# Kernel optimization log

Hardware: AMD Instinct MI355X
Metric: run time of the kernel (lower is better)

## Reference

```python
import jax, jax.numpy as jnp
import numpy as np

NUM_TOKENS = 4096
LATENT_DIM = 128
BETA = 0.25
TEMP = 1.0  # temperature buffer (eval mode, no annealing)


def _l2_normalize(x, eps=1e-12):
    n = jnp.linalg.norm(x, axis=-1, keepdims=True)
    return x / jnp.maximum(n, eps)


def setup_inputs() -> dict:
    key = jax.random.key(0)
    k1, k2 = jax.random.split(key)
    latent = jax.random.normal(k1, (16, 1024, LATENT_DIM), dtype=jnp.float32)
    # codebook init: uniform(-1/num_tokens, 1/num_tokens) as in the module
    codebook_w = jax.random.uniform(
        k2, (NUM_TOKENS, LATENT_DIM), dtype=jnp.float32,
        minval=-1.0 / NUM_TOKENS, maxval=1.0 / NUM_TOKENS)
    return {"latent": latent, "codebook_w": codebook_w}


def reference(latent, codebook_w):
    B, S, D = latent.shape
    K = codebook_w.shape[0]
    flat = latent.reshape(-1, D)                      # [N, D]
    N = flat.shape[0]

    # cosine similarity between normalized inputs and codes
    cos = _l2_normalize(flat) @ _l2_normalize(codebook_w).T  # [N, K]

    # squared euclidean distances
    dist = (jnp.sum(flat * flat, axis=1, keepdims=True)
            - 2.0 * (flat @ codebook_w.T)
            + jnp.sum(codebook_w * codebook_w, axis=1))       # [N, K]

    soft = jax.nn.softmax(-dist / max(TEMP, 1e-5), axis=-1)   # [N, K]
    idx = jnp.argmax(soft, axis=-1)                            # [N]
    hard = jax.nn.one_hot(idx, K, dtype=flat.dtype)            # [N, K]
    # straight-through assignment
    assign = hard + soft - jax.lax.stop_gradient(soft)

    sel_cos = jnp.take_along_axis(cos, idx[:, None], axis=1).mean()

    # codebook self pairwise euclidean distances (K x K)
    sq = jnp.sum(codebook_w * codebook_w, axis=1)
    d2 = sq[:, None] + sq[None, :] - 2.0 * (codebook_w @ codebook_w.T)
    d = jnp.sqrt(jnp.maximum(d2, 0.0))
    # diagonal is exactly 0 after clamp, so off-diagonal mean = sum/(K*(K-1))
    avg_euclidean = d.sum() / (K * (K - 1))
    min_euclidean = jnp.min(jnp.where(jnp.eye(K, dtype=bool), jnp.inf, d))

    quantized = (assign @ codebook_w).reshape(B, S, D)
    commitment_loss = BETA * jnp.mean((jax.lax.stop_gradient(latent) - quantized) ** 2)
    codebook_loss = jnp.mean((latent - jax.lax.stop_gradient(quantized)) ** 2)
    quantized_st = latent + jax.lax.stop_gradient(quantized - latent)

    avg_probs = hard.mean(axis=0)
    perplexity = jnp.exp(-jnp.sum(avg_probs * jnp.log(avg_probs + 1e-10)))

    return (quantized_st, idx, commitment_loss, codebook_loss,
            perplexity, sel_cos, avg_euclidean, min_euclidean)
```

## Files before the change

### kernel.cpp

```cpp
#include <hip/hip_runtime.h>
#include <hip/hip_fp16.h>
#include <math.h>

#define NTOK 16384
#define KCB  4096
#define DIM  128
#define NG8  (KCB / 8)

typedef short bf16x8 __attribute__((ext_vector_type(8)));
typedef float f32x4  __attribute__((ext_vector_type(4)));

static __device__ inline unsigned short rne_bf16(float f) {
  unsigned u = __float_as_uint(f);
  return (unsigned short)((u + 0x7FFFu + ((u >> 16) & 1u)) >> 16);
}


__global__ __launch_bounds__(256) void k_prep(const float* __restrict__ lat,
                                              const float* __restrict__ cb,
                                              float* __restrict__ sumx2,
                                              float* __restrict__ sumc2,
                                              float* __restrict__ absum,
                                              int* __restrict__ cnt,
                                              unsigned short* __restrict__ cbh) {
  if (blockIdx.x < (NTOK + KCB) / 4) {
    if (blockIdx.x < 16) cnt[blockIdx.x * 256 + threadIdx.x] = 0;
    const int row  = blockIdx.x * 4 + (threadIdx.x >> 6);
    const int lane = threadIdx.x & 63;
    const float* src = (row < NTOK) ? (lat + (size_t)row * DIM)
                                    : (cb + (size_t)(row - NTOK) * DIM);
    float2 v = *(const float2*)(src + lane * 2);
    double s  = (double)v.x * (double)v.x + (double)v.y * (double)v.y;
    double sa = fabs((double)v.x) + fabs((double)v.y);
#pragma unroll
    for (int m = 32; m >= 1; m >>= 1) {
      s  += __shfl_xor(s, m, 64);
      sa += __shfl_xor(sa, m, 64);
    }
    if (lane == 0) {
      if (row < NTOK) { sumx2[row] = (float)s; absum[row] = (float)sa; }
      else            sumc2[row - NTOK] = (float)s;
    }
  } else {
    const int b = blockIdx.x - (NTOK + KCB) / 4;
    const int base = (b * 256 + threadIdx.x) * 8;
    float4 v0 = *(const float4*)(cb + base);
    float4 v1 = *(const float4*)(cb + base + 4);
    ushort4 o0, o1;
    o0.x = rne_bf16(v0.x); o0.y = rne_bf16(v0.y); o0.z = rne_bf16(v0.z); o0.w = rne_bf16(v0.w);
    o1.x = rne_bf16(v1.x); o1.y = rne_bf16(v1.y); o1.z = rne_bf16(v1.z); o1.w = rne_bf16(v1.w);
    *(ushort4*)(cbh + base) = o0;
    *(ushort4*)(cbh + base + 4) = o1;
  }
}

__global__ __launch_bounds__(256) void k_approx(const float* __restrict__ lat,
                                                const unsigned short* __restrict__ cbh,
                                                unsigned short* __restrict__ gmax8) {
  __shared__ __align__(16) unsigned char smem[16384];
  __shared__ __align__(16) unsigned short gbuf[256][36];
  const int t = threadIdx.x;
  const int w = t >> 6, l = t & 63;
  const int l15 = l & 15, lq = l >> 4;
  const int tokb = blockIdx.x * 256 + w * 64;
  const int ct0 = blockIdx.y * 4;

  bf16x8 bfr[4][4];
#pragma unroll
  for (int ctile = 0; ctile < 4; ++ctile) {
    const float* row = lat + (size_t)(tokb + ctile * 16 + l15) * DIM;
#pragma unroll
    for (int ks = 0; ks < 4; ++ks) {
      const int d0 = ks * 32 + lq * 4;
      float4 c0 = *(const float4*)(row + d0);
      float4 c1 = *(const float4*)(row + d0 + 16);
      union { ushort4 u4[2]; bf16x8 v; } cv;
      cv.u4[0].x = rne_bf16(c0.x); cv.u4[0].y = rne_bf16(c0.y);
      cv.u4[0].z = rne_bf16(c0.z); cv.u4[0].w = rne_bf16(c0.w);
      cv.u4[1].x = rne_bf16(c1.x); cv.u4[1].y = rne_bf16(c1.y);
      cv.u4[1].z = rne_bf16(c1.z); cv.u4[1].w = rne_bf16(c1.w);
      bfr[ctile][ks] = cv.v;
    }
  }

  for (int it = 0; it < 4; ++it) {
    const int ct = ct0 + it;
    __syncthreads();
    {
      const int r = t & 63, seg = t >> 6;
      const unsigned short* src = cbh + (size_t)(ct * 64 + r) * DIM + seg * 32;
      const int sw = (r & 7) << 4;
#pragma unroll
      for (int i = 0; i < 4; ++i) {
        uint4 v = *(const uint4*)(src + i * 8);
        *(uint4*)(smem + r * 256 + ((seg * 64 + i * 16) ^ sw)) = v;
      }
    }
    __syncthreads();

#pragma unroll
    for (int rt = 0; rt < 4; ++rt) {
      const int row = rt * 16 + l15;
      const int sw = (row & 7) << 4;
      bf16x8 afr[4];
#pragma unroll
      for (int ks = 0; ks < 4; ++ks) {
        const int off = ks * 64 + lq * 8;
        union { uint2 u2[2]; bf16x8 v; } cv;
        cv.u2[0] = *(const uint2*)(smem + row * 256 + (off ^ sw));
        cv.u2[1] = *(const uint2*)(smem + row * 256 + (((off + 32)) ^ sw));
        afr[ks] = cv.v;
      }
      f32x4 acc[4];
#pragma unroll
      for (int c = 0; c < 4; ++c) acc[c] = (f32x4){0.0f, 0.0f, 0.0f, 0.0f};
#pragma unroll
      for (int ks = 0; ks < 4; ++ks)
#pragma unroll
        for (int c = 0; c < 4; ++c)
          acc[c] = __builtin_amdgcn_mfma_f32_16x16x32_bf16(afr[ks], bfr[c][ks], acc[c], 0, 0, 0);
#pragma unroll
      for (int c = 0; c < 4; ++c) {
        float gm = fmaxf(fmaxf(acc[c][0], acc[c][1]), fmaxf(acc[c][2], acc[c][3]));
        gm = fmaxf(gm, __shfl_xor(gm, 16, 64));
        if ((lq & 1) == 0) {
          const int tokl = w * 64 + c * 16 + l15;
          gbuf[tokl][it * 8 + rt * 2 + (lq >> 1)] =
              __half_as_ushort(__float2half(gm));
        }
      }
    }
  }

  __syncthreads();
  for (int c = t; c < 1024; c += 256) {
    const int token = c >> 2, seg = c & 3;
    uint2 a = *(const uint2*)(&gbuf[token][seg * 8]);
    uint2 b = *(const uint2*)(&gbuf[token][seg * 8 + 4]);
    uint4 o = make_uint4(a.x, a.y, b.x, b.y);
    *(uint4*)(gmax8 + (size_t)(blockIdx.x * 256 + token) * NG8 +
              blockIdx.y * 32 + seg * 8) = o;
  }
}

__global__ __launch_bounds__(256) void k_resolve_pair(
    const float* __restrict__ lat,
    const float* __restrict__ cb,
    const float* __restrict__ sumx2,
    const float* __restrict__ sumc2,
    const float* __restrict__ absum,
    const unsigned short* __restrict__ gmax8,
    const unsigned short* __restrict__ cbh,
    float* __restrict__ qout,
    float* __restrict__ idx_out,
    float* __restrict__ msum,
    float* __restrict__ csum,
    int* __restrict__ cnt,
    float* __restrict__ pairsum,
    float* __restrict__ pairmin) {
  __shared__ __align__(16) unsigned char pool[16640];

  if (blockIdx.x < 1024) {
    const int f = blockIdx.x;
    const int bx = f & 15, by = f >> 4;
    unsigned char* smem = pool;
    float* qs = (float*)(pool + 16384);
    const int t = threadIdx.x;
    const int w = t >> 6, l = t & 63;
    const int l15 = l & 15, lq = l >> 4;
    const int jb = bx * 256 + w * 64;
    const int kb = by * 64;

    {
      const int r = t & 63, seg = t >> 6;
      const unsigned short* src = cbh + (size_t)(kb + r) * DIM + seg * 32;
      const int sw = (r & 7) << 4;
#pragma unroll
      for (int i = 0; i < 4; ++i) {
        uint4 v = *(const uint4*)(src + i * 8);
        *(uint4*)(smem + r * 256 + ((seg * 64 + i * 16) ^ sw)) = v;
      }
      if (t < 64) qs[t] = sumc2[kb + t];
    }

    bf16x8 bfr[4][4];
    float qj[4];
#pragma unroll
    for (int ct = 0; ct < 4; ++ct) {
      const unsigned short* rh = cbh + (size_t)(jb + ct * 16 + l15) * DIM;
#pragma unroll
      for (int ks = 0; ks < 4; ++ks) {
        const int d0 = ks * 32 + lq * 4;
        union { ushort4 u4[2]; bf16x8 v; } cvv;
        cvv.u4[0] = *(const ushort4*)(rh + d0);
        cvv.u4[1] = *(const ushort4*)(rh + d0 + 16);
        bfr[ct][ks] = cvv.v;
      }
      qj[ct] = sumc2[jb + ct * 16 + l15];
    }
    __syncthreads();

    float lsum = 0.0f, lmin = INFINITY;

#pragma unroll
    for (int rt = 0; rt < 4; ++rt) {
      const int row = rt * 16 + l15;
      const int sw = (row & 7) << 4;
      bf16x8 afr[4];
#pragma unroll
      for (int ks = 0; ks < 4; ++ks) {
        const int off = ks * 64 + lq * 8;
        union { uint2 u2[2]; bf16x8 v; } cv;
        cv.u2[0] = *(const uint2*)(smem + row * 256 + (off ^ sw));
        cv.u2[1] = *(const uint2*)(smem + row * 256 + (((off + 32)) ^ sw));
        afr[ks] = cv.v;
      }
      f32x4 acc[4];
#pragma unroll
      for (int c = 0; c < 4; ++c) acc[c] = (f32x4){0.0f, 0.0f, 0.0f, 0.0f};
#pragma unroll
      for (int ks = 0; ks < 4; ++ks)
#pragma unroll
        for (int c = 0; c < 4; ++c)
          acc[c] = __builtin_amdgcn_mfma_f32_16x16x32_bf16(afr[ks], bfr[c][ks], acc[c], 0, 0, 0);

#pragma unroll
      for (int c = 0; c < 4; ++c) {
        const int jg = jb + c * 16 + l15;
#pragma unroll
        for (int reg = 0; reg < 4; ++reg) {
          const int krl = rt * 16 + lq * 4 + reg;
          const int kg = kb + krl;
          const float d2 = (qj[c] + qs[krl]) - 2.0f * acc[c][reg];
          const float dd = sqrtf(fmaxf(d2, 0.0f));
          lsum += dd;
          if (jg != kg) lmin = fminf(lmin, dd);
        }
      }
    }

#pragma unroll
    for (int s = 32; s >= 1; s >>= 1) {
      lsum += __shfl_xor(lsum, s, 64);
      lmin = fminf(lmin, __shfl_xor(lmin, s, 64));
    }
    if (l == 0) {
      const int slot = f * 4 + w;
      pairsum[slot] = lsum;
      pairmin[slot] = lmin;
    }
  } else {
    const int bid = blockIdx.x - 1024;
    float (*xs)[DIM] = (float (*)[DIM])pool;
    unsigned short (*q)[NG8] = (unsigned short (*)[NG8])(pool + 2048);
    const int w = threadIdx.x >> 6, l = threadIdx.x & 63;
    const int tok = bid * 4 + w;

    const float2 xv = *(const float2*)(lat + (size_t)tok * DIM + l * 2);
    const uint4 hv = *(const uint4*)(gmax8 + (size_t)tok * NG8 + l * 8);
    const float sx = sumx2[tok];
    const float ab = absum[tok];
    *(float2*)(&xs[w][l * 2]) = xv;

    float hf[8];
    hf[0] = __half2float(__ushort_as_half((unsigned short)(hv.x & 0xFFFFu)));
    hf[1] = __half2float(__ushort_as_half((unsigned short)(hv.x >> 16)));
    hf[2] = __half2float(__ushort_as_half((unsigned short)(hv.y & 0xFFFFu)));
    hf[3] = __half2float(__ushort_as_half((unsigned short)(hv.y >> 16)));
    hf[4] = __half2float(__ushort_as_half((unsigned short)(hv.z & 0xFFFFu)));
    hf[5] = __half2float(__ushort_as_half((unsigned short)(hv.z >> 16)));
    hf[6] = __half2float(__ushort_as_half((unsigned short)(hv.w & 0xFFFFu)));
    hf[7] = __half2float(__ushort_as_half((unsigned short)(hv.w >> 16)));
    float m = hf[0];
#pragma unroll
    for (int i = 1; i < 8; ++i) m = fmaxf(m, hf[i]);
#pragma unroll
    for (int s = 32; s >= 1; s >>= 1) m = fmaxf(m, __shfl_xor(m, s, 64));
    const float thr = m - (ab * 3.8224e-6f + 6.0e-5f);

    const unsigned long long ltm = (1ull << l) - 1ull;
    int n = 0;
#pragma unroll
    for (int i = 0; i < 8; ++i) {
      const bool f2 = (hf[i] >= thr);
      const unsigned long long b = __ballot(f2);
      if (f2) q[w][n + __popcll(b & ltm)] = (unsigned short)(l * 8 + i);
      n += __popcll(b);
    }

    const int slot = l >> 3, cidx = l & 7;
    unsigned long long bestp = ~0ull;
    const float4* xr4 = (const float4*)xs[w];

    for (int base = 0; base < n; base += 8) {
      unsigned long long pack = ~0ull;
      const int qi = base + slot;
      if (qi < n) {
        const int g = (int)q[w][qi];
        const int code = g * 8 + cidx;
        const float4* crow = (const float4*)(cb + (size_t)code * DIM);
        float acc = 0.0f;
#pragma unroll 8
        for (int ch = 0; ch < 32; ++ch) {
          const float4 c = crow[ch];
          const float4 x = xr4[ch];
          acc = fmaf(x.x, c.x, acc); acc = fmaf(x.y, c.y, acc);
          acc = fmaf(x.z, c.z, acc); acc = fmaf(x.w, c.w, acc);
        }
        const float dist = (sx - 2.0f * acc) + sumc2[code];
        pack = ((unsigned long long)__float_as_uint(dist) << 32) | (unsigned)code;
      }
#pragma unroll
      for (int s = 32; s >= 1; s >>= 1) {
        const unsigned long long o = __shfl_xor(pack, s, 64);
        pack = (o < pack) ? o : pack;
      }
      bestp = (pack < bestp) ? pack : bestp;
    }

    const int code = (int)(bestp & 0xFFFFFFFFull);
    const float2 c2 = *(const float2*)(cb + (size_t)code * DIM + l * 2);
    const float o0 = xv.x + (c2.x - xv.x);
    const float o1 = xv.y + (c2.y - xv.y);
    *(float2*)(qout + (size_t)tok * DIM + l * 2) = make_float2(o0, o1);
    const float e0 = xv.x - c2.x, e1 = xv.y - c2.y;
    float msel = e0 * e0 + e1 * e1;
    float dt = xv.x * c2.x + xv.y * c2.y;
#pragma unroll
    for (int s = 32; s >= 1; s >>= 1) {
      msel += __shfl_xor(msel, s, 64);
      dt += __shfl_xor(dt, s, 64);
    }
    if (l == 0) {
      const float nx = fmaxf(sqrtf(sx), 1e-12f);
      const float nc = fmaxf(sqrtf(sumc2[code]), 1e-12f);
      msum[tok] = msel;
      csum[tok] = dt / (nx * nc);
      idx_out[tok] = (float)code;
      atomicAdd(&cnt[code], 1);
    }
  }
}

__global__ __launch_bounds__(1024) void k_final(const int* __restrict__ cnt,
                                                const float* __restrict__ msum,
                                                const float* __restrict__ csum,
                                                const float* __restrict__ pairsum,
                                                const float* __restrict__ pairmin,
                                                float* __restrict__ outs) {
  __shared__ float sh[1024], sh2[1024], sh3[1024], sh4[1024];
  const int t = threadIdx.x;
  float ent = 0.0f;
  for (int k = t; k < KCB; k += 1024) {
    const float p = (float)cnt[k] * (1.0f / (float)NTOK);
    ent += p * logf(p + 1e-10f);
  }
  float ms = 0.0f, cs = 0.0f;
  for (int i = t; i < NTOK; i += 1024) { ms += msum[i]; cs += csum[i]; }
  float ps = 0.0f, pm = INFINITY;
  for (int i = t; i < 4096; i += 1024) { ps += pairsum[i]; pm = fminf(pm, pairmin[i]); }

  sh[t] = ent; sh2[t] = ms; sh3[t] = cs; sh4[t] = ps;
  __syncthreads();
  for (int s = 512; s >= 1; s >>= 1) {
    if (t < s) { sh[t] += sh[t + s]; sh2[t] += sh2[t + s];
                 sh3[t] += sh3[t + s]; sh4[t] += sh4[t + s]; }
    __syncthreads();
  }
  const float ent_tot = sh[0];
  const float ms_tot  = sh2[0];
  const float cs_tot  = sh3[0];
  const float ps_tot  = sh4[0];
  __syncthreads();
  sh[t] = pm;
  __syncthreads();
  for (int s = 512; s >= 1; s >>= 1) {
    if (t < s) sh[t] = fminf(sh[t], sh[t + s]);
    __syncthreads();
  }
  if (t == 0) {
    const float mse = ms_tot * (1.0f / (float)(NTOK * DIM));
    outs[0] = 0.25f * mse;
    outs[1] = mse;
    outs[2] = expf(-ent_tot);
    outs[3] = cs_tot * (1.0f / (float)NTOK);
    outs[4] = ps_tot / ((float)KCB * (float)(KCB - 1));
    outs[5] = sh[0];
  }
}

extern "C" void kernel_launch(void* const* d_in, const int* in_sizes, int n_in,
                              void* d_out, int out_size, void* d_ws, size_t ws_size,
                              hipStream_t stream) {
  const float* lat = (const float*)d_in[0];
  const float* cb  = (const float*)d_in[1];

  float* out     = (float*)d_out;
  float* qout    = out;
  float* idx_out = out + (size_t)NTOK * DIM;
  float* outs    = idx_out + NTOK;

  float* W        = (float*)d_ws;
  float* sumx2    = W;
  float* sumc2    = sumx2 + NTOK;
  float* absum    = sumc2 + KCB;
  int*   cnt      = (int*)(absum + NTOK);
  float* msum     = (float*)(cnt + KCB);
  float* csum     = msum + NTOK;
  float* pairsum  = csum + NTOK;
  float* pairmin  = pairsum + 4096;
  unsigned short* cbh   = (unsigned short*)(pairmin + 4096);
  unsigned short* gmax8 = cbh + (size_t)KCB * DIM;

  hipLaunchKernelGGL(k_prep, dim3((NTOK + KCB) / 4 + KCB * DIM / (256 * 8)),
                     dim3(256), 0, stream, lat, cb, sumx2, sumc2, absum, cnt, cbh);
  hipLaunchKernelGGL(k_approx, dim3(NTOK / 256, 16), dim3(256), 0, stream,
                     lat, cbh, gmax8);
  hipLaunchKernelGGL(k_resolve_pair, dim3(1024 + NTOK / 4), dim3(256), 0, stream,
                     lat, cb, sumx2, sumc2, absum, gmax8, cbh,
                     qout, idx_out, msum, csum, cnt, pairsum, pairmin);
  hipLaunchKernelGGL(k_final, dim3(1), dim3(1024), 0, stream, cnt,
                     msum, csum, pairsum, pairmin, outs);
}
```

Measured before the change: 120.4 us.

## Fuse prep and approx kernels, convert codebook to bf16 on the fly

Merges the norm/prep kernel and the bf16 approximate-scan kernel into one launch, with the norm blocks appended after the 1024 MFMA scan blocks. The separate bf16 codebook copy (cbh) is dropped; both the scan and the resolve/pair kernels now read the fp32 codebook and round to bf16 while staging into shared memory or registers. This removes one kernel launch, the dependency barrier between prep and scan, and a codebook write and read. The cost is twice the global bytes per codebook load plus repeated conversion ALU work in every block.

```diff
diff --git a/kernel.cpp b/kernel.cpp
--- a/kernel.cpp
+++ b/kernel.cpp
@@ -16,16 +16,109 @@
 }
 
 
-__global__ __launch_bounds__(256) void k_prep(const float* __restrict__ lat,
+__global__ __launch_bounds__(256) void k_scan(const float* __restrict__ lat,
                                               const float* __restrict__ cb,
                                               float* __restrict__ sumx2,
                                               float* __restrict__ sumc2,
                                               float* __restrict__ absum,
                                               int* __restrict__ cnt,
-                                              unsigned short* __restrict__ cbh) {
-  if (blockIdx.x < (NTOK + KCB) / 4) {
-    if (blockIdx.x < 16) cnt[blockIdx.x * 256 + threadIdx.x] = 0;
-    const int row  = blockIdx.x * 4 + (threadIdx.x >> 6);
+                                              unsigned short* __restrict__ gmax8) {
+  __shared__ __align__(16) unsigned char smem[16384];
+  __shared__ __align__(16) unsigned short gbuf[256][36];
+  if (blockIdx.x < 1024) {
+    const int xb = blockIdx.x & 63, yb = blockIdx.x >> 6;
+    const int t = threadIdx.x;
+    const int w = t >> 6, l = t & 63;
+    const int l15 = l & 15, lq = l >> 4;
+    const int tokb = xb * 256 + w * 64;
+    const int ct0 = yb * 4;
+
+    bf16x8 bfr[4][4];
+#pragma unroll
+    for (int ctile = 0; ctile < 4; ++ctile) {
+      const float* row = lat + (size_t)(tokb + ctile * 16 + l15) * DIM;
+#pragma unroll
+      for (int ks = 0; ks < 4; ++ks) {
+        const int d0 = ks * 32 + lq * 4;
+        float4 c0 = *(const float4*)(row + d0);
+        float4 c1 = *(const float4*)(row + d0 + 16);
+        union { ushort4 u4[2]; bf16x8 v; } cv;
+        cv.u4[0].x = rne_bf16(c0.x); cv.u4[0].y = rne_bf16(c0.y);
+        cv.u4[0].z = rne_bf16(c0.z); cv.u4[0].w = rne_bf16(c0.w);
+        cv.u4[1].x = rne_bf16(c1.x); cv.u4[1].y = rne_bf16(c1.y);
+        cv.u4[1].z = rne_bf16(c1.z); cv.u4[1].w = rne_bf16(c1.w);
+        bfr[ctile][ks] = cv.v;
+      }
+    }
+
+    for (int it = 0; it < 4; ++it) {
+      const int ct = ct0 + it;
+      __syncthreads();
+      {
+        const int r = t & 63, seg = t >> 6;
+        const float* src = cb + (size_t)(ct * 64 + r) * DIM + seg * 32;
+        const int sw = (r & 7) << 4;
+#pragma unroll
+        for (int i = 0; i < 4; ++i) {
+          float4 a = *(const float4*)(src + i * 8);
+          float4 b = *(const float4*)(src + i * 8 + 4);
+          union { unsigned short s[8]; uint4 v; } pk;
+          pk.s[0] = rne_bf16(a.x); pk.s[1] = rne_bf16(a.y);
+          pk.s[2] = rne_bf16(a.z); pk.s[3] = rne_bf16(a.w);
+          pk.s[4] = rne_bf16(b.x); pk.s[5] = rne_bf16(b.y);
+          pk.s[6] = rne_bf16(b.z); pk.s[7] = rne_bf16(b.w);
+          *(uint4*)(smem + r * 256 + ((seg * 64 + i * 16) ^ sw)) = pk.v;
+        }
+      }
+      __syncthreads();
+
+#pragma unroll
+      for (int rt = 0; rt < 4; ++rt) {
+        const int row = rt * 16 + l15;
+        const int sw = (row & 7) << 4;
+        bf16x8 afr[4];
+#pragma unroll
+        for (int ks = 0; ks < 4; ++ks) {
+          const int off = ks * 64 + lq * 8;
+          union { uint2 u2[2]; bf16x8 v; } cv;
+          cv.u2[0] = *(const uint2*)(smem + row * 256 + (off ^ sw));
+          cv.u2[1] = *(const uint2*)(smem + row * 256 + (((off + 32)) ^ sw));
+          afr[ks] = cv.v;
+        }
+        f32x4 acc[4];
+#pragma unroll
+        for (int c = 0; c < 4; ++c) acc[c] = (f32x4){0.0f, 0.0f, 0.0f, 0.0f};
+#pragma unroll
+        for (int ks = 0; ks < 4; ++ks)
+#pragma unroll
+          for (int c = 0; c < 4; ++c)
+            acc[c] = __builtin_amdgcn_mfma_f32_16x16x32_bf16(afr[ks], bfr[c][ks], acc[c], 0, 0, 0);
+#pragma unroll
+        for (int c = 0; c < 4; ++c) {
+          float gm = fmaxf(fmaxf(acc[c][0], acc[c][1]), fmaxf(acc[c][2], acc[c][3]));
+          gm = fmaxf(gm, __shfl_xor(gm, 16, 64));
+          if ((lq & 1) == 0) {
+            const int tokl = w * 64 + c * 16 + l15;
+            gbuf[tokl][it * 8 + rt * 2 + (lq >> 1)] =
+                __half_as_ushort(__float2half(gm));
+          }
+        }
+      }
+    }
+
+    __syncthreads();
+    for (int c = t; c < 1024; c += 256) {
+      const int token = c >> 2, seg = c & 3;
+      uint2 a = *(const uint2*)(&gbuf[token][seg * 8]);
+      uint2 b = *(const uint2*)(&gbuf[token][seg * 8 + 4]);
+      uint4 o = make_uint4(a.x, a.y, b.x, b.y);
+      *(uint4*)(gmax8 + (size_t)(xb * 256 + token) * NG8 +
+                yb * 32 + seg * 8) = o;
+    }
+  } else {
+    const int rb = blockIdx.x - 1024;
+    if (rb < 16) cnt[rb * 256 + threadIdx.x] = 0;
+    const int row  = rb * 4 + (threadIdx.x >> 6);
     const int lane = threadIdx.x & 63;
     const float* src = (row < NTOK) ? (lat + (size_t)row * DIM)
                                     : (cb + (size_t)(row - NTOK) * DIM);
@@ -41,105 +134,6 @@
       if (row < NTOK) { sumx2[row] = (float)s; absum[row] = (float)sa; }
       else            sumc2[row - NTOK] = (float)s;
     }
-  } else {
-    const int b = blockIdx.x - (NTOK + KCB) / 4;
-    const int base = (b * 256 + threadIdx.x) * 8;
-    float4 v0 = *(const float4*)(cb + base);
-    float4 v1 = *(const float4*)(cb + base + 4);
-    ushort4 o0, o1;
-    o0.x = rne_bf16(v0.x); o0.y = rne_bf16(v0.y); o0.z = rne_bf16(v0.z); o0.w = rne_bf16(v0.w);
-    o1.x = rne_bf16(v1.x); o1.y = rne_bf16(v1.y); o1.z = rne_bf16(v1.z); o1.w = rne_bf16(v1.w);
-    *(ushort4*)(cbh + base) = o0;
-    *(ushort4*)(cbh + base + 4) = o1;
-  }
-}
-
-__global__ __launch_bounds__(256) void k_approx(const float* __restrict__ lat,
-                                                const unsigned short* __restrict__ cbh,
-                                                unsigned short* __restrict__ gmax8) {
-  __shared__ __align__(16) unsigned char smem[16384];
-  __shared__ __align__(16) unsigned short gbuf[256][36];
-  const int t = threadIdx.x;
-  const int w = t >> 6, l = t & 63;
-  const int l15 = l & 15, lq = l >> 4;
-  const int tokb = blockIdx.x * 256 + w * 64;
-  const int ct0 = blockIdx.y * 4;
-
-  bf16x8 bfr[4][4];
-#pragma unroll
-  for (int ctile = 0; ctile < 4; ++ctile) {
-    const float* row = lat + (size_t)(tokb + ctile * 16 + l15) * DIM;
-#pragma unroll
-    for (int ks = 0; ks < 4; ++ks) {
-      const int d0 = ks * 32 + lq * 4;
-      float4 c0 = *(const float4*)(row + d0);
-      float4 c1 = *(const float4*)(row + d0 + 16);
-      union { ushort4 u4[2]; bf16x8 v; } cv;
-      cv.u4[0].x = rne_bf16(c0.x); cv.u4[0].y = rne_bf16(c0.y);
-      cv.u4[0].z = rne_bf16(c0.z); cv.u4[0].w = rne_bf16(c0.w);
-      cv.u4[1].x = rne_bf16(c1.x); cv.u4[1].y = rne_bf16(c1.y);
-      cv.u4[1].z = rne_bf16(c1.z); cv.u4[1].w = rne_bf16(c1.w);
-      bfr[ctile][ks] = cv.v;
-    }
-  }
-
-  for (int it = 0; it < 4; ++it) {
-    const int ct = ct0 + it;
-    __syncthreads();
-    {
-      const int r = t & 63, seg = t >> 6;
-      const unsigned short* src = cbh + (size_t)(ct * 64 + r) * DIM + seg * 32;
-      const int sw = (r & 7) << 4;
-#pragma unroll
-      for (int i = 0; i < 4; ++i) {
-        uint4 v = *(const uint4*)(src + i * 8);
-        *(uint4*)(smem + r * 256 + ((seg * 64 + i * 16) ^ sw)) = v;
-      }
-    }
-    __syncthreads();
-
-#pragma unroll
-    for (int rt = 0; rt < 4; ++rt) {
-      const int row = rt * 16 + l15;
-      const int sw = (row & 7) << 4;
-      bf16x8 afr[4];
-#pragma unroll
-      for (int ks = 0; ks < 4; ++ks) {
-        const int off = ks * 64 + lq * 8;
-        union { uint2 u2[2]; bf16x8 v; } cv;
-        cv.u2[0] = *(const uint2*)(smem + row * 256 + (off ^ sw));
-        cv.u2[1] = *(const uint2*)(smem + row * 256 + (((off + 32)) ^ sw));
-        afr[ks] = cv.v;
-      }
-      f32x4 acc[4];
-#pragma unroll
-      for (int c = 0; c < 4; ++c) acc[c] = (f32x4){0.0f, 0.0f, 0.0f, 0.0f};
-#pragma unroll
-      for (int ks = 0; ks < 4; ++ks)
-#pragma unroll
-        for (int c = 0; c < 4; ++c)
-          acc[c] = __builtin_amdgcn_mfma_f32_16x16x32_bf16(afr[ks], bfr[c][ks], acc[c], 0, 0, 0);
-#pragma unroll
-      for (int c = 0; c < 4; ++c) {
-        float gm = fmaxf(fmaxf(acc[c][0], acc[c][1]), fmaxf(acc[c][2], acc[c][3]));
-        gm = fmaxf(gm, __shfl_xor(gm, 16, 64));
-        if ((lq & 1) == 0) {
-          const int tokl = w * 64 + c * 16 + l15;
-          gbuf[tokl][it * 8 + rt * 2 + (lq >> 1)] =
-              __half_as_ushort(__float2half(gm));
-        }
-      }
-    }
-  }
-
-  __syncthreads();
-  for (int c = t; c < 1024; c += 256) {
-    const int token = c >> 2, seg = c & 3;
-    uint2 a = *(const uint2*)(&gbuf[token][seg * 8]);
-    uint2 b = *(const uint2*)(&gbuf[token][seg * 8 + 4]);
-    uint4 o = make_uint4(a.x, a.y, b.x, b.y);
-    *(uint4*)(gmax8 + (size_t)(blockIdx.x * 256 + token) * NG8 +
-              blockIdx.y * 32 + seg * 8) = o;
   }
 }
 
@@ -150,7 +144,6 @@
     const float* __restrict__ sumc2,
     const float* __restrict__ absum,
     const unsigned short* __restrict__ gmax8,
-    const unsigned short* __restrict__ cbh,
     float* __restrict__ qout,
     float* __restrict__ idx_out,
     float* __restrict__ msum,
@@ -173,12 +166,18 @@
 
     {
       const int r = t & 63, seg = t >> 6;
-      const unsigned short* src = cbh + (size_t)(kb + r) * DIM + seg * 32;
+      const float* src = cb + (size_t)(kb + r) * DIM + seg * 32;
       const int sw = (r & 7) << 4;
 #pragma unroll
       for (int i = 0; i < 4; ++i) {
-        uint4 v = *(const uint4*)(src + i * 8);
-        *(uint4*)(smem + r * 256 + ((seg * 64 + i * 16) ^ sw)) = v;
+        float4 a = *(const float4*)(src + i * 8);
+        float4 b = *(const float4*)(src + i * 8 + 4);
+        union { unsigned short s[8]; uint4 v; } pk;
+        pk.s[0] = rne_bf16(a.x); pk.s[1] = rne_bf16(a.y);
+        pk.s[2] = rne_bf16(a.z); pk.s[3] = rne_bf16(a.w);
+        pk.s[4] = rne_bf16(b.x); pk.s[5] = rne_bf16(b.y);
+        pk.s[6] = rne_bf16(b.z); pk.s[7] = rne_bf16(b.w);
+        *(uint4*)(smem + r * 256 + ((seg * 64 + i * 16) ^ sw)) = pk.v;
       }
       if (t < 64) qs[t] = sumc2[kb + t];
     }
@@ -187,14 +186,18 @@
     float qj[4];
 #pragma unroll
     for (int ct = 0; ct < 4; ++ct) {
-      const unsigned short* rh = cbh + (size_t)(jb + ct * 16 + l15) * DIM;
+      const float* rh = cb + (size_t)(jb + ct * 16 + l15) * DIM;
 #pragma unroll
       for (int ks = 0; ks < 4; ++ks) {
         const int d0 = ks * 32 + lq * 4;
-        union { ushort4 u4[2]; bf16x8 v; } cvv;
-        cvv.u4[0] = *(const ushort4*)(rh + d0);
-        cvv.u4[1] = *(const ushort4*)(rh + d0 + 16);
-        bfr[ct][ks] = cvv.v;
+        float4 c0 = *(const float4*)(rh + d0);
+        float4 c1 = *(const float4*)(rh + d0 + 16);
+        union { ushort4 u4[2]; bf16x8 v; } cv;
+        cv.u4[0].x = rne_bf16(c0.x); cv.u4[0].y = rne_bf16(c0.y);
+        cv.u4[0].z = rne_bf16(c0.z); cv.u4[0].w = rne_bf16(c0.w);
+        cv.u4[1].x = rne_bf16(c1.x); cv.u4[1].y = rne_bf16(c1.y);
+        cv.u4[1].z = rne_bf16(c1.z); cv.u4[1].w = rne_bf16(c1.w);
+        bfr[ct][ks] = cv.v;
       }
       qj[ct] = sumc2[jb + ct * 16 + l15];
     }
@@ -409,15 +412,12 @@
   float* csum     = msum + NTOK;
   float* pairsum  = csum + NTOK;
   float* pairmin  = pairsum + 4096;
-  unsigned short* cbh   = (unsigned short*)(pairmin + 4096);
-  unsigned short* gmax8 = cbh + (size_t)KCB * DIM;
-
-  hipLaunchKernelGGL(k_prep, dim3((NTOK + KCB) / 4 + KCB * DIM / (256 * 8)),
-                     dim3(256), 0, stream, lat, cb, sumx2, sumc2, absum, cnt, cbh);
-  hipLaunchKernelGGL(k_approx, dim3(NTOK / 256, 16), dim3(256), 0, stream,
-                     lat, cbh, gmax8);
+  unsigned short* gmax8 = (unsigned short*)(pairmin + 4096);
+
+  hipLaunchKernelGGL(k_scan, dim3(1024 + (NTOK + KCB) / 4), dim3(256), 0, stream,
+                     lat, cb, sumx2, sumc2, absum, cnt, gmax8);
   hipLaunchKernelGGL(k_resolve_pair, dim3(1024 + NTOK / 4), dim3(256), 0, stream,
-                     lat, cb, sumx2, sumc2, absum, gmax8, cbh,
+                     lat, cb, sumx2, sumc2, absum, gmax8,
                      qout, idx_out, msum, csum, cnt, pairsum, pairmin);
   hipLaunchKernelGGL(k_final, dim3(1), dim3(1024), 0, stream, cnt,
                      msum, csum, pairsum, pairmin, outs);
```

New measurement: 140.6 us. +16.7%, slower.
